# Optimization experiments

Measured on AMD Instinct MI355X. Metric: run time of the kernel, lower is better.

## Reference

```python
import jax, jax.numpy as jnp
import numpy as np

B, S, H, DH = 2, 4096, 8, 64
D = H * DH


def setup_inputs() -> dict:
    key = jax.random.key(0)
    ks = jax.random.split(key, 6)
    std = 1.0 / np.sqrt(D)
    return {
        "x": jax.random.normal(ks[0], (B, S, D), dtype=jnp.float32),
        "Wq": jax.random.normal(ks[1], (D, D), dtype=jnp.float32) * std,
        "Wk": jax.random.normal(ks[2], (D, D), dtype=jnp.float32) * std,
        "Wv": jax.random.normal(ks[3], (D, D), dtype=jnp.float32) * std,
        "Wo": jax.random.normal(ks[4], (D, D), dtype=jnp.float32) * std,
        "bo": jnp.zeros((D,), dtype=jnp.float32),
    }


def reference(x, Wq, Wk, Wv, Wo, bo):
    scale = DH ** (-0.5)
    # torch Linear: y = x @ W.T
    q = x @ Wq.T  # [B,S,D]
    k = x @ Wk.T
    v = x @ Wv.T
    # split heads -> [B,H,S,Dh]
    q = q.reshape(B, S, H, DH).transpose(0, 2, 1, 3)
    k = k.reshape(B, S, H, DH).transpose(0, 2, 1, 3)
    v = v.reshape(B, S, H, DH).transpose(0, 2, 1, 3)
    score = jnp.einsum('bhqd,bhkd->bhqk', q, k) * scale  # [B,H,S,S]
    weights = jax.nn.softmax(score, axis=-1)
    attn = jnp.einsum('bhqk,bhkd->bhqd', weights, v)  # [B,H,S,Dh]
    h_ = attn.transpose(0, 2, 1, 3).reshape(B, S, D)
    return h_ @ Wo.T + bo
```

## Files before the change

### kernel.cpp

```cpp
#include <hip/hip_runtime.h>

#define LOG2E 1.44269504088896340736f

typedef unsigned short u16;
typedef __bf16 bf16x4_t __attribute__((ext_vector_type(4)));
typedef __bf16 bf16x8_t __attribute__((ext_vector_type(8)));
typedef float f32x4_t __attribute__((ext_vector_type(4)));

__device__ __forceinline__ f32x4_t mfma16(bf16x8_t a, bf16x8_t b, f32x4_t c) {
  return __builtin_amdgcn_mfma_f32_16x16x32_bf16(a, b, c, 0, 0, 0);
}

__device__ __forceinline__ void gl_lds16(const u16* g, u16* l) {
  __builtin_amdgcn_global_load_lds(
      (const __attribute__((address_space(1))) unsigned int*)g,
      (__attribute__((address_space(3))) unsigned int*)l, 16, 0, 0);
}

__global__ __launch_bounds__(256) void cast_kernel(
    const float* __restrict__ x, const float* __restrict__ Wq, const float* __restrict__ Wk,
    const float* __restrict__ Wv, const float* __restrict__ Wo,
    u16* __restrict__ Xb, u16* __restrict__ Wqb, u16* __restrict__ Wkb,
    u16* __restrict__ Wvb, u16* __restrict__ Wob) {
  const int bid = blockIdx.x;
  const float* src;
  u16* dst;
  float scale = 1.f;
  int rel;
  if (bid < 2048)      { src = x;  dst = Xb;  rel = bid; }
  else if (bid < 2176) { src = Wq; dst = Wqb; rel = bid - 2048; scale = 0.125f * LOG2E; }
  else if (bid < 2304) { src = Wk; dst = Wkb; rel = bid - 2176; }
  else if (bid < 2432) { src = Wv; dst = Wvb; rel = bid - 2304; }
  else                 { src = Wo; dst = Wob; rel = bid - 2432; }
  const int i = rel * 2048 + threadIdx.x * 8;
  f32x4_t a = *(const f32x4_t*)(src + i) * scale;
  f32x4_t b = *(const f32x4_t*)(src + i + 4) * scale;
  union { uint4 u; struct { bf16x4_t lo, hi; } s; } c;
  c.s.lo = __builtin_convertvector(a, bf16x4_t);
  c.s.hi = __builtin_convertvector(b, bf16x4_t);
  *(uint4*)(dst + i) = c.u;
}

template <int MODE>
__device__ __forceinline__ void gemm_core_bf16(const u16* __restrict__ A, const u16* __restrict__ Bt,
                                               void* __restrict__ Cout, const float* __restrict__ bo,
                                               int Mbase, int Nbase) {
  __shared__ __align__(16) u16 smem[128 * 128];
  u16 (*As)[64] = (u16(*)[64])smem;
  u16 (*Bs)[64] = (u16(*)[64])(smem + 128 * 64);
  const int t = threadIdx.x;
  const int wave = t >> 6, lane = t & 63;
  const int r = lane & 15, qd = lane >> 4;
  const int wm = wave & 1, wn = wave >> 1;
  const int rr = lane >> 3;
  const int s8 = ((lane & 7) ^ (rr & 7)) * 8;

  f32x4_t acc[4][4];
#pragma unroll
  for (int i = 0; i < 4; i++)
#pragma unroll
    for (int j = 0; j < 4; j++) { f32x4_t z = {0.f, 0.f, 0.f, 0.f}; acc[i][j] = z; }

  const u16* pa = A  + (Mbase + wave * 32 + rr) * 512 + s8;
  const u16* pb = Bt + (Nbase + wave * 32 + rr) * 512 + s8;
  u16* la = &As[wave * 32][0];
  u16* lb = &Bs[wave * 32][0];

  for (int k0 = 0; k0 < 512; k0 += 64) {
#pragma unroll
    for (int j = 0; j < 4; j++) gl_lds16(pa + k0 + j * 8 * 512, la + j * 8 * 64);
#pragma unroll
    for (int j = 0; j < 4; j++) gl_lds16(pb + k0 + j * 8 * 512, lb + j * 8 * 64);
    __syncthreads();
#pragma unroll
    for (int h = 0; h < 2; h++) {
      bf16x8_t af[4], bfr[4];
#pragma unroll
      for (int i = 0; i < 4; i++)
        af[i]  = *(const bf16x8_t*)&As[wm * 64 + i * 16 + r][((h * 4 + qd) ^ (r & 7)) * 8];
#pragma unroll
      for (int j = 0; j < 4; j++)
        bfr[j] = *(const bf16x8_t*)&Bs[wn * 64 + j * 16 + r][((h * 4 + qd) ^ (r & 7)) * 8];
#pragma unroll
      for (int i = 0; i < 4; i++)
#pragma unroll
        for (int j = 0; j < 4; j++) acc[i][j] = mfma16(af[i], bfr[j], acc[i][j]);
    }
    __syncthreads();
  }

  if (MODE != 2) {
#pragma unroll
    for (int i = 0; i < 4; i++)
#pragma unroll
      for (int j = 0; j < 4; j++)
#pragma unroll
        for (int reg = 0; reg < 4; reg++) {
          int row = wm * 64 + i * 16 + qd * 4 + reg;
          int col = wn * 64 + j * 16 + r;
          __bf16 bv = (__bf16)acc[i][j][reg];
          smem[row * 128 + (col ^ (((row >> 2) & 7) << 3))] = *(u16*)&bv;
        }
    __syncthreads();
#pragma unroll
    for (int p = 0; p < 8; p++) {
      int row = p * 16 + (t >> 4);
      int col = (t & 15) * 8;
      uint4 v = *(const uint4*)&smem[row * 128 + (col ^ (((row >> 2) & 7) << 3))];
      if (MODE == 0) {
        *(uint4*)&((u16*)Cout)[(Mbase + row) * 512 + Nbase + col] = v;
      } else {
        int bb = Nbase >> 12;
        int ss = (Nbase & 4095) + col;
        *(uint4*)&((u16*)Cout)[((long)(bb * 512 + Mbase + row)) * 4096 + ss] = v;
      }
    }
  } else {
    float* stf = (float*)smem;
    float bv[4];
#pragma unroll
    for (int j = 0; j < 4; j++) bv[j] = bo[Nbase + wn * 64 + j * 16 + r];
#pragma unroll
    for (int hh = 0; hh < 2; hh++) {
      __syncthreads();
      if (wm == hh) {
#pragma unroll
        for (int i = 0; i < 4; i++)
#pragma unroll
          for (int j = 0; j < 4; j++)
#pragma unroll
            for (int reg = 0; reg < 4; reg++) {
              int row = i * 16 + qd * 4 + reg;
              int col = wn * 64 + j * 16 + r;
              stf[row * 128 + (col ^ (((row >> 2) & 7) << 2))] = acc[i][j][reg] + bv[j];
            }
      }
      __syncthreads();
#pragma unroll
      for (int p = 0; p < 4; p++) {
        int row = p * 16 + (t >> 4);
        int col = (t & 15) * 8;
        f32x4_t v0 = *(const f32x4_t*)&stf[row * 128 + ((col) ^ (((row >> 2) & 7) << 2))];
        f32x4_t v1 = *(const f32x4_t*)&stf[row * 128 + ((col + 4) ^ (((row >> 2) & 7) << 2))];
        *(f32x4_t*)&((float*)Cout)[(Mbase + hh * 64 + row) * 512 + Nbase + col] = v0;
        *(f32x4_t*)&((float*)Cout)[(Mbase + hh * 64 + row) * 512 + Nbase + col + 4] = v1;
      }
    }
  }
}

__global__ __launch_bounds__(256) void gemm_qkv_kernel(
    const u16* __restrict__ Xb,
    const u16* __restrict__ Wqb, const u16* __restrict__ Wkb, const u16* __restrict__ Wvb,
    u16* __restrict__ Q, u16* __restrict__ K, u16* __restrict__ Vt) {
  if (blockIdx.z == 0)
    gemm_core_bf16<0>(Xb, Wqb, Q, nullptr, blockIdx.x * 128, blockIdx.y * 128);
  else if (blockIdx.z == 1)
    gemm_core_bf16<0>(Xb, Wkb, K, nullptr, blockIdx.x * 128, blockIdx.y * 128);
  else
    gemm_core_bf16<1>(Wvb, Xb, Vt, nullptr, blockIdx.y * 128, blockIdx.x * 128);
}

__global__ __launch_bounds__(256) void gemm_out_kernel(
    const u16* __restrict__ Aat, const u16* __restrict__ Wob,
    float* __restrict__ Out, const float* __restrict__ bo) {
  gemm_core_bf16<2>(Aat, Wob, Out, bo, blockIdx.x * 128, blockIdx.y * 128);
}

__global__ __launch_bounds__(256, 2) void attn_kernel(
    const u16* __restrict__ Q, const u16* __restrict__ K, const u16* __restrict__ Vt,
    u16* __restrict__ Oattn) {
  __shared__ __align__(16) u16 Ks[2][2][4096];
  __shared__ __align__(16) u16 Vs[2][2][4096];

  const int t = threadIdx.x;
  const int wave = t >> 6, lane = t & 63;
  const int r = lane & 15, qd = lane >> 4;
  const int g = wave & 1, kv = wave >> 1;
  const int bh = blockIdx.y;
  const int b = bh >> 3, h = bh & 7;
  const long bbase = (long)b * 4096 * 512;
  const int q0 = blockIdx.x * 128;

  const int sw = r & 7;
  const int ck0 = (qd ^ sw) * 8;
  const int ck1 = ((qd + 4) ^ sw) * 8;
  int vo0[2], vo1[2];
#pragma unroll
  for (int c = 0; c < 2; c++) {
    vo0[c] = ((c * 4 + (qd >> 1)) ^ sw) * 8 + 4 * (qd & 1);
    vo1[c] = ((c * 4 + 2 + (qd >> 1)) ^ sw) * 8 + 4 * (qd & 1);
  }

  bf16x8_t ones8;
#pragma unroll
  for (int j = 0; j < 8; j++) ones8[j] = (__bf16)1.0f;

  bf16x8_t qf[4][2];
#pragma unroll
  for (int qa = 0; qa < 4; qa++) {
    const u16* qp = Q + bbase + (long)(q0 + g * 64 + qa * 16 + r) * 512 + h * 64 + qd * 8;
    qf[qa][0] = *(const bf16x8_t*)(qp);
    qf[qa][1] = *(const bf16x8_t*)(qp + 32);
  }

  f32x4_t accO[4][4];
  f32x4_t accL[4];
#pragma unroll
  for (int qa = 0; qa < 4; qa++) {
    f32x4_t z = {0.f, 0.f, 0.f, 0.f};
    accL[qa] = z;
#pragma unroll
    for (int nt = 0; nt < 4; nt++) accO[qa][nt] = z;
  }

  const int rr = lane >> 3;
  const int cc = (lane & 7) ^ rr;
  const u16* kgb = K + bbase + (long)(kv * 2048 + g * 32 + rr) * 512 + h * 64 + cc * 8;
  const u16* vgb = Vt + ((long)(b * 512 + h * 64 + g * 32 + rr)) * 4096 + kv * 2048 + cc * 8;

#pragma unroll
  for (int i = 0; i < 4; i++) gl_lds16(kgb + (long)i * 8 * 512, &Ks[kv][0][g * 2048] + i * 512);
#pragma unroll
  for (int i = 0; i < 4; i++) gl_lds16(vgb + i * 8 * 4096, &Vs[kv][0][g * 2048] + i * 512);

  for (int it = 0; it < 32; it++) {
    const int buf = it & 1;
    __syncthreads();

    if (it < 31) {
      const int nb = (it + 1) & 1;
      const long ko = (long)(it + 1) * 64;
#pragma unroll
      for (int i = 0; i < 4; i++)
        gl_lds16(kgb + (ko + i * 8) * 512, &Ks[kv][nb][g * 2048] + i * 512);
#pragma unroll
      for (int i = 0; i < 4; i++)
        gl_lds16(vgb + ko + (long)i * 8 * 4096, &Vs[kv][nb][g * 2048] + i * 512);
    }

    bf16x8_t kf[4][2];
#pragma unroll
    for (int nt = 0; nt < 4; nt++) {
      const u16* kb = &Ks[kv][buf][(nt * 16 + r) * 64];
      kf[nt][0] = *(const bf16x8_t*)(kb + ck0);
      kf[nt][1] = *(const bf16x8_t*)(kb + ck1);
    }

    f32x4_t St[4][4];
    __builtin_amdgcn_s_setprio(1);
#pragma unroll
    for (int qa = 0; qa < 4; qa++)
#pragma unroll
      for (int nt = 0; nt < 4; nt++) {
        f32x4_t z = {0.f, 0.f, 0.f, 0.f};
        z = mfma16(kf[nt][0], qf[qa][0], z);
        z = mfma16(kf[nt][1], qf[qa][1], z);
        St[qa][nt] = z;
      }
    __builtin_amdgcn_s_setprio(0);

    bf16x8_t pf[4][2];
#pragma unroll
    for (int qa = 0; qa < 4; qa++)
#pragma unroll
      for (int c = 0; c < 2; c++) {
        f32x4_t e0, e1;
#pragma unroll
        for (int j = 0; j < 4; j++) {
          e0[j] = __builtin_amdgcn_exp2f(St[qa][2 * c][j]);
          e1[j] = __builtin_amdgcn_exp2f(St[qa][2 * c + 1][j]);
        }
        bf16x4_t b0 = __builtin_convertvector(e0, bf16x4_t);
        bf16x4_t b1 = __builtin_convertvector(e1, bf16x4_t);
        bf16x8_t p8;
#pragma unroll
        for (int j = 0; j < 4; j++) { p8[j] = b0[j]; p8[4 + j] = b1[j]; }
        pf[qa][c] = p8;
      }

#pragma unroll
    for (int qa = 0; qa < 4; qa++)
#pragma unroll
      for (int c = 0; c < 2; c++)
        accL[qa] = mfma16(ones8, pf[qa][c], accL[qa]);

#pragma unroll
    for (int c = 0; c < 2; c++) {
      bf16x8_t va[4];
#pragma unroll
      for (int dm = 0; dm < 4; dm++) {
        const u16* vb = &Vs[kv][buf][(dm * 16 + r) * 64];
        union { uint4 u; bf16x8_t v; } cat;
        *(uint2*)&cat.u.x = *(const uint2*)(vb + vo0[c]);
        *(uint2*)&cat.u.z = *(const uint2*)(vb + vo1[c]);
        va[dm] = cat.v;
      }
      __builtin_amdgcn_s_setprio(1);
#pragma unroll
      for (int qa = 0; qa < 4; qa++)
#pragma unroll
        for (int dm = 0; dm < 4; dm++)
          accO[qa][dm] = mfma16(va[dm], pf[qa][c], accO[qa][dm]);
      __builtin_amdgcn_s_setprio(0);
    }
  }

  __syncthreads();
  float* Sc  = (float*)&Ks[0][0][0];
  float* Lsc = (float*)&Vs[0][0][0];
  if (kv == 1) {
#pragma unroll
    for (int qa = 0; qa < 4; qa++) {
#pragma unroll
      for (int dm = 0; dm < 4; dm++)
        *(f32x4_t*)&Sc[g * 4096 + ((qa * 4 + dm) * 64 + lane) * 4] = accO[qa][dm];
      Lsc[g * 256 + qa * 64 + lane] = accL[qa][0];
    }
  }
  __syncthreads();
  if (kv == 0) {
#pragma unroll
    for (int qa = 0; qa < 4; qa++) {
      float L = accL[qa][0] + Lsc[g * 256 + qa * 64 + lane];
      float inv = 1.f / L;
      int gq = q0 + g * 64 + qa * 16 + r;
#pragma unroll
      for (int dm = 0; dm < 4; dm++) {
        f32x4_t o = *(const f32x4_t*)&Sc[g * 4096 + ((qa * 4 + dm) * 64 + lane) * 4];
        o += accO[qa][dm];
        bf16x4_t ob;
#pragma unroll
        for (int reg = 0; reg < 4; reg++) ob[reg] = (__bf16)(o[reg] * inv);
        *(uint2*)&Oattn[bbase + (long)gq * 512 + h * 64 + dm * 16 + qd * 4] = *(uint2*)&ob;
      }
    }
  }
}

extern "C" void kernel_launch(void* const* d_in, const int* in_sizes, int n_in,
                              void* d_out, int out_size, void* d_ws, size_t ws_size,
                              hipStream_t stream) {
  const float* x  = (const float*)d_in[0];
  const float* Wq = (const float*)d_in[1];
  const float* Wk = (const float*)d_in[2];
  const float* Wv = (const float*)d_in[3];
  const float* Wo = (const float*)d_in[4];
  const float* bo = (const float*)d_in[5];
  float* out = (float*)d_out;

  u16* ws  = (u16*)d_ws;
  u16* Qb  = ws;
  u16* Kb  = Qb  + 4194304;
  u16* Vtg = Kb  + 4194304;
  u16* Ab  = Vtg + 4194304;
  u16* Xb  = Ab;
  u16* Wqb = Ab  + 4194304;
  u16* Wkb = Wqb + 262144;
  u16* Wvb = Wkb + 262144;
  u16* Wob = Wvb + 262144;

  cast_kernel<<<2560, 256, 0, stream>>>(x, Wq, Wk, Wv, Wo, Xb, Wqb, Wkb, Wvb, Wob);

  dim3 g1(64, 4, 3);
  gemm_qkv_kernel<<<g1, 256, 0, stream>>>(Xb, Wqb, Wkb, Wvb, Qb, Kb, Vtg);

  dim3 g2(32, 16);
  attn_kernel<<<g2, 256, 0, stream>>>(Qb, Kb, Vtg, Ab);

  dim3 g3(64, 4);
  gemm_out_kernel<<<g3, 256, 0, stream>>>(Ab, Wob, out, bo);
}
```

Measured before the change: 189.9 us.

## Enlarge attention blocks to 256 queries and remap blocks per XCD

The attention kernel now runs 512 threads (8 waves) per block, so each block covers 256 queries. Each staged K/V tile is shared by twice as many queries, which halves the global-to-LDS traffic per query. Block indices are also remapped so that blocks with the same batch-head land on the same XCD, which is meant to improve L2 reuse of K and V. The LDS is reorganised into one flat buffer plus a separate row-sum array. The cost is a tighter register budget: with launch_bounds(512,2) there may not be enough VGPRs for the large accumulator and fragment arrays, which could cause spills. The grid also shrinks to 256 blocks.

```diff
diff --git a/kernel.cpp b/kernel.cpp
--- a/kernel.cpp
+++ b/kernel.cpp
@@ -167,20 +167,26 @@
   gemm_core_bf16<2>(Aat, Wob, Out, bo, blockIdx.x * 128, blockIdx.y * 128);
 }
 
-__global__ __launch_bounds__(256, 2) void attn_kernel(
+__global__ __launch_bounds__(512, 2) void attn_kernel(
     const u16* __restrict__ Q, const u16* __restrict__ K, const u16* __restrict__ Vt,
     u16* __restrict__ Oattn) {
-  __shared__ __align__(16) u16 Ks[2][2][4096];
-  __shared__ __align__(16) u16 Vs[2][2][4096];
+  __shared__ __align__(16) u16 KVs[32768];
+  __shared__ float Lsc2[1024];
+#define KS(kvv, bf) (KVs + ((kvv) * 2 + (bf)) * 4096)
+#define VS(kvv, bf) (KVs + 16384 + ((kvv) * 2 + (bf)) * 4096)
 
   const int t = threadIdx.x;
   const int wave = t >> 6, lane = t & 63;
   const int r = lane & 15, qd = lane >> 4;
-  const int g = wave & 1, kv = wave >> 1;
-  const int bh = blockIdx.y;
+  const int g = wave >> 1, kv = wave & 1;
+
+  const int flat = blockIdx.y * 16 + blockIdx.x;
+  const int xcd = flat & 7, idx = flat >> 3;
+  const int bh = xcd * 2 + (idx >> 4);
+  const int qi = idx & 15;
   const int b = bh >> 3, h = bh & 7;
   const long bbase = (long)b * 4096 * 512;
-  const int q0 = blockIdx.x * 128;
+  const int q0 = qi * 256;
 
   const int sw = r & 7;
   const int ck0 = (qd ^ sw) * 8;
@@ -216,13 +222,13 @@
 
   const int rr = lane >> 3;
   const int cc = (lane & 7) ^ rr;
-  const u16* kgb = K + bbase + (long)(kv * 2048 + g * 32 + rr) * 512 + h * 64 + cc * 8;
-  const u16* vgb = Vt + ((long)(b * 512 + h * 64 + g * 32 + rr)) * 4096 + kv * 2048 + cc * 8;
-
-#pragma unroll
-  for (int i = 0; i < 4; i++) gl_lds16(kgb + (long)i * 8 * 512, &Ks[kv][0][g * 2048] + i * 512);
-#pragma unroll
-  for (int i = 0; i < 4; i++) gl_lds16(vgb + i * 8 * 4096, &Vs[kv][0][g * 2048] + i * 512);
+  const u16* kgb = K + bbase + (long)(kv * 2048 + g * 16 + rr) * 512 + h * 64 + cc * 8;
+  const u16* vgb = Vt + ((long)(b * 512 + h * 64 + g * 16 + rr)) * 4096 + kv * 2048 + cc * 8;
+
+#pragma unroll
+  for (int i = 0; i < 2; i++) gl_lds16(kgb + (long)i * 8 * 512, KS(kv, 0) + g * 1024 + i * 512);
+#pragma unroll
+  for (int i = 0; i < 2; i++) gl_lds16(vgb + (long)i * 8 * 4096, VS(kv, 0) + g * 1024 + i * 512);
 
   for (int it = 0; it < 32; it++) {
     const int buf = it & 1;
@@ -232,17 +238,17 @@
       const int nb = (it + 1) & 1;
       const long ko = (long)(it + 1) * 64;
 #pragma unroll
-      for (int i = 0; i < 4; i++)
-        gl_lds16(kgb + (ko + i * 8) * 512, &Ks[kv][nb][g * 2048] + i * 512);
-#pragma unroll
-      for (int i = 0; i < 4; i++)
-        gl_lds16(vgb + ko + (long)i * 8 * 4096, &Vs[kv][nb][g * 2048] + i * 512);
+      for (int i = 0; i < 2; i++)
+        gl_lds16(kgb + (ko + i * 8) * 512, KS(kv, nb) + g * 1024 + i * 512);
+#pragma unroll
+      for (int i = 0; i < 2; i++)
+        gl_lds16(vgb + ko + (long)i * 8 * 4096, VS(kv, nb) + g * 1024 + i * 512);
     }
 
     bf16x8_t kf[4][2];
 #pragma unroll
     for (int nt = 0; nt < 4; nt++) {
-      const u16* kb = &Ks[kv][buf][(nt * 16 + r) * 64];
+      const u16* kb = KS(kv, buf) + (nt * 16 + r) * 64;
       kf[nt][0] = *(const bf16x8_t*)(kb + ck0);
       kf[nt][1] = *(const bf16x8_t*)(kb + ck1);
     }
@@ -290,7 +296,7 @@
       bf16x8_t va[4];
 #pragma unroll
       for (int dm = 0; dm < 4; dm++) {
-        const u16* vb = &Vs[kv][buf][(dm * 16 + r) * 64];
+        const u16* vb = VS(kv, buf) + (dm * 16 + r) * 64;
         union { uint4 u; bf16x8_t v; } cat;
         *(uint2*)&cat.u.x = *(const uint2*)(vb + vo0[c]);
         *(uint2*)&cat.u.z = *(const uint2*)(vb + vo1[c]);
@@ -307,22 +313,21 @@
   }
 
   __syncthreads();
-  float* Sc  = (float*)&Ks[0][0][0];
-  float* Lsc = (float*)&Vs[0][0][0];
+  float* Sc = (float*)KVs;
   if (kv == 1) {
 #pragma unroll
     for (int qa = 0; qa < 4; qa++) {
 #pragma unroll
       for (int dm = 0; dm < 4; dm++)
         *(f32x4_t*)&Sc[g * 4096 + ((qa * 4 + dm) * 64 + lane) * 4] = accO[qa][dm];
-      Lsc[g * 256 + qa * 64 + lane] = accL[qa][0];
+      Lsc2[g * 256 + qa * 64 + lane] = accL[qa][0];
     }
   }
   __syncthreads();
   if (kv == 0) {
 #pragma unroll
     for (int qa = 0; qa < 4; qa++) {
-      float L = accL[qa][0] + Lsc[g * 256 + qa * 64 + lane];
+      float L = accL[qa][0] + Lsc2[g * 256 + qa * 64 + lane];
       float inv = 1.f / L;
       int gq = q0 + g * 64 + qa * 16 + r;
 #pragma unroll
@@ -336,6 +341,8 @@
       }
     }
   }
+#undef KS
+#undef VS
 }
 
 extern "C" void kernel_launch(void* const* d_in, const int* in_sizes, int n_in,
@@ -365,8 +372,8 @@
   dim3 g1(64, 4, 3);
   gemm_qkv_kernel<<<g1, 256, 0, stream>>>(Xb, Wqb, Wkb, Wvb, Qb, Kb, Vtg);
 
-  dim3 g2(32, 16);
-  attn_kernel<<<g2, 256, 0, stream>>>(Qb, Kb, Vtg, Ab);
+  dim3 g2(16, 16);
+  attn_kernel<<<g2, 512, 0, stream>>>(Qb, Kb, Vtg, Ab);
 
   dim3 g3(64, 4);
   gemm_out_kernel<<<g3, 256, 0, stream>>>(Ab, Wob, out, bo);
```

New measurement: 192.3 us. Within noise of the previous version (+1.3%).

## Fuse Q/K/V projections into one GEMM kernel sharing the X tile

Applied to the files above, without the earlier changes.

Replaces the three-way z-split QKV GEMM with one 512-thread kernel. Each block loads the X tile once and multiplies it against Wq, Wk and Wv tiles held together in LDS. This removes the triple reload of X and cuts the block count to 256. In exchange it uses more LDS and registers per block (24 accumulators per lane) and single-buffered loads, and V is written transposed through an LDS staging pass. Parallelism drops from 768 blocks to 256, which may leave some CUs idle.

```diff
diff --git a/kernel.cpp b/kernel.cpp
--- a/kernel.cpp
+++ b/kernel.cpp
@@ -41,6 +41,124 @@
   *(uint4*)(dst + i) = c.u;
 }
 
+__global__ __launch_bounds__(512) void gemm_qkv_fused(
+    const u16* __restrict__ Xb,
+    const u16* __restrict__ Wqb, const u16* __restrict__ Wkb, const u16* __restrict__ Wvb,
+    u16* __restrict__ Q, u16* __restrict__ K, u16* __restrict__ Vt) {
+  __shared__ __align__(16) u16 SM[32768];
+  u16 (*As)[64] = (u16(*)[64])SM;
+  u16 (*Bq)[64] = (u16(*)[64])(SM + 8192);
+  u16 (*Bk)[64] = (u16(*)[64])(SM + 16384);
+  u16 (*Bv)[64] = (u16(*)[64])(SM + 24576);
+  const int t = threadIdx.x;
+  const int wave = t >> 6, lane = t & 63;
+  const int r = lane & 15, qd = lane >> 4;
+  const int wm = wave & 1, wn = wave >> 1;
+  const int rr = lane >> 3;
+  const int s8 = ((lane & 7) ^ (rr & 7)) * 8;
+  const int Mbase = blockIdx.x * 128, Nbase = blockIdx.y * 128;
+
+  f32x4_t acc[3][4][2];
+#pragma unroll
+  for (int w = 0; w < 3; w++)
+#pragma unroll
+    for (int i = 0; i < 4; i++)
+#pragma unroll
+      for (int j = 0; j < 2; j++) { f32x4_t z = {0.f, 0.f, 0.f, 0.f}; acc[w][i][j] = z; }
+
+  const u16* pa = Xb  + (Mbase + wave * 16 + rr) * 512 + s8;
+  const u16* pq = Wqb + (Nbase + wave * 16 + rr) * 512 + s8;
+  const u16* pk = Wkb + (Nbase + wave * 16 + rr) * 512 + s8;
+  const u16* pv = Wvb + (Nbase + wave * 16 + rr) * 512 + s8;
+  u16* la = &As[wave * 16][0];
+  u16* lq = &Bq[wave * 16][0];
+  u16* lk = &Bk[wave * 16][0];
+  u16* lv = &Bv[wave * 16][0];
+
+  for (int k0 = 0; k0 < 512; k0 += 64) {
+#pragma unroll
+    for (int p = 0; p < 2; p++) {
+      gl_lds16(pa + k0 + p * 8 * 512, la + p * 512);
+      gl_lds16(pq + k0 + p * 8 * 512, lq + p * 512);
+      gl_lds16(pk + k0 + p * 8 * 512, lk + p * 512);
+      gl_lds16(pv + k0 + p * 8 * 512, lv + p * 512);
+    }
+    __syncthreads();
+#pragma unroll
+    for (int h = 0; h < 2; h++) {
+      bf16x8_t af[4];
+#pragma unroll
+      for (int i = 0; i < 4; i++)
+        af[i] = *(const bf16x8_t*)&As[wm * 64 + i * 16 + r][((h * 4 + qd) ^ (r & 7)) * 8];
+      bf16x8_t fq[2], fk[2], fv[2];
+#pragma unroll
+      for (int j = 0; j < 2; j++) {
+        fq[j] = *(const bf16x8_t*)&Bq[wn * 32 + j * 16 + r][((h * 4 + qd) ^ (r & 7)) * 8];
+        fk[j] = *(const bf16x8_t*)&Bk[wn * 32 + j * 16 + r][((h * 4 + qd) ^ (r & 7)) * 8];
+        fv[j] = *(const bf16x8_t*)&Bv[wn * 32 + j * 16 + r][((h * 4 + qd) ^ (r & 7)) * 8];
+      }
+#pragma unroll
+      for (int i = 0; i < 4; i++)
+#pragma unroll
+        for (int j = 0; j < 2; j++) {
+          acc[0][i][j] = mfma16(af[i], fq[j], acc[0][i][j]);
+          acc[1][i][j] = mfma16(af[i], fk[j], acc[1][i][j]);
+          acc[2][i][j] = mfma16(af[i], fv[j], acc[2][i][j]);
+        }
+    }
+    __syncthreads();
+  }
+
+  const int erow = t >> 4;
+  const int ecol = (t & 15) * 8;
+#pragma unroll
+  for (int w = 0; w < 2; w++) {
+    __syncthreads();
+    u16* dst = (w == 0) ? Q : K;
+#pragma unroll
+    for (int i = 0; i < 4; i++)
+#pragma unroll
+      for (int j = 0; j < 2; j++)
+#pragma unroll
+        for (int reg = 0; reg < 4; reg++) {
+          int row = wm * 64 + i * 16 + qd * 4 + reg;
+          int col = wn * 32 + j * 16 + r;
+          __bf16 bvv = (__bf16)acc[w][i][j][reg];
+          SM[row * 128 + (col ^ (((row >> 2) & 7) << 3))] = *(u16*)&bvv;
+        }
+    __syncthreads();
+#pragma unroll
+    for (int p = 0; p < 4; p++) {
+      int row = p * 32 + erow;
+      uint4 v = *(const uint4*)&SM[row * 128 + (ecol ^ (((row >> 2) & 7) << 3))];
+      *(uint4*)&dst[(Mbase + row) * 512 + Nbase + ecol] = v;
+    }
+  }
+  __syncthreads();
+#pragma unroll
+  for (int i = 0; i < 4; i++)
+#pragma unroll
+    for (int j = 0; j < 2; j++)
+#pragma unroll
+      for (int reg = 0; reg < 4; reg++) {
+        int srow = wm * 64 + i * 16 + qd * 4 + reg;
+        int dcol = wn * 32 + j * 16 + r;
+        __bf16 bvv = (__bf16)acc[2][i][j][reg];
+        SM[dcol * 128 + (srow ^ (((dcol >> 2) & 7) << 3))] = *(u16*)&bvv;
+      }
+  __syncthreads();
+  {
+    const int bb = Mbase >> 12;
+    const int smod = Mbase & 4095;
+#pragma unroll
+    for (int p = 0; p < 4; p++) {
+      int d = p * 32 + erow;
+      uint4 v = *(const uint4*)&SM[d * 128 + (ecol ^ (((d >> 2) & 7) << 3))];
+      *(uint4*)&Vt[((long)(bb * 512 + Nbase + d)) * 4096 + smod + ecol] = v;
+    }
+  }
+}
+
 template <int MODE>
 __device__ __forceinline__ void gemm_core_bf16(const u16* __restrict__ A, const u16* __restrict__ Bt,
                                                void* __restrict__ Cout, const float* __restrict__ bo,
@@ -149,18 +267,6 @@
   }
 }
 
-__global__ __launch_bounds__(256) void gemm_qkv_kernel(
-    const u16* __restrict__ Xb,
-    const u16* __restrict__ Wqb, const u16* __restrict__ Wkb, const u16* __restrict__ Wvb,
-    u16* __restrict__ Q, u16* __restrict__ K, u16* __restrict__ Vt) {
-  if (blockIdx.z == 0)
-    gemm_core_bf16<0>(Xb, Wqb, Q, nullptr, blockIdx.x * 128, blockIdx.y * 128);
-  else if (blockIdx.z == 1)
-    gemm_core_bf16<0>(Xb, Wkb, K, nullptr, blockIdx.x * 128, blockIdx.y * 128);
-  else
-    gemm_core_bf16<1>(Wvb, Xb, Vt, nullptr, blockIdx.y * 128, blockIdx.x * 128);
-}
-
 __global__ __launch_bounds__(256) void gemm_out_kernel(
     const u16* __restrict__ Aat, const u16* __restrict__ Wob,
     float* __restrict__ Out, const float* __restrict__ bo) {
@@ -362,8 +468,8 @@
 
   cast_kernel<<<2560, 256, 0, stream>>>(x, Wq, Wk, Wv, Wo, Xb, Wqb, Wkb, Wvb, Wob);
 
-  dim3 g1(64, 4, 3);
-  gemm_qkv_kernel<<<g1, 256, 0, stream>>>(Xb, Wqb, Wkb, Wvb, Qb, Kb, Vtg);
+  dim3 g1(64, 4);
+  gemm_qkv_fused<<<g1, 512, 0, stream>>>(Xb, Wqb, Wkb, Wvb, Qb, Kb, Vtg);
 
   dim3 g2(32, 16);
   attn_kernel<<<g2, 256, 0, stream>>>(Qb, Kb, Vtg, Ab);
```

New measurement: 180.2 us. 1.05x faster.
